# Performance work log

Measured on AMD Instinct MI355X. Metric: run time of the kernel, lower is better.

The kernel has to match this reference:

```python
import jax, jax.numpy as jnp
import numpy as np

B, T, DIM = 4, 2048, 1024
H, DH = 16, 64  # num_heads, dim_head; weight_dim = H*DH = 1024
SCALE = DIM ** (-0.5)  # note: original scales by dim**-0.5, not dim_head**-0.5


def setup_inputs() -> dict:
    key = jax.random.key(0)
    k1, k2, k3 = jax.random.split(key, 3)
    x = jax.random.normal(k1, (B, T, DIM), dtype=jnp.float32)
    w_qkv = jax.random.normal(k2, (3 * H * DH, DIM), dtype=jnp.float32) * (DIM ** -0.5)
    w_out = jax.random.normal(k3, (DIM, H * DH), dtype=jnp.float32) * ((H * DH) ** -0.5)
    b_out = jnp.zeros((DIM,), dtype=jnp.float32)
    return {"x": x, "w_qkv": w_qkv, "w_out": w_out, "b_out": b_out}


def reference(x, w_qkv, w_out, b_out):
    # qkv: [b, t, 3*H*DH] (torch Linear: x @ W^T)
    qkv = jnp.einsum('btc,oc->bto', x, w_qkv)
    # rearrange 'b t (d k h) -> k b h t d' with k=3, h=H: d is the OUTERMOST
    # factor of the flattened axis, then k, then h (h fastest-varying).
    qkv = qkv.reshape(B, T, DH, 3, H)          # [b, t, d, k, h]
    qkv = jnp.transpose(qkv, (3, 0, 4, 1, 2))   # [k, b, h, t, d]
    q, k, v = qkv[0], qkv[1], qkv[2]
    # scores: [b, h, t, t]
    attn = jnp.einsum('bhid,bhjd->bhij', q, k) * SCALE
    attn = jax.nn.softmax(attn, axis=-1)
    out = jnp.einsum('bhij,bhjd->bhid', attn, v)           # [b, h, t, d]
    out = jnp.transpose(out, (0, 2, 1, 3)).reshape(B, T, H * DH)  # 'b h t d -> b t (h d)'
    return jnp.einsum('btc,oc->bto', out, w_out) + b_out
```

## Files before the change

### kernel.cpp

```cpp
#include <hip/hip_runtime.h>
#include <hip/hip_bf16.h>


typedef __attribute__((ext_vector_type(8))) short short8;
typedef __attribute__((ext_vector_type(4))) float floatx4;

static __device__ __forceinline__ floatx4 mfma16(short8 a, short8 b, floatx4 c) {
    return __builtin_amdgcn_mfma_f32_16x16x32_bf16(a, b, c, 0, 0, 0);
}

static __device__ __forceinline__ unsigned short f2bf_bits(float f) {
    __hip_bfloat16 h = __float2bfloat16(f);
    return *reinterpret_cast<unsigned short*>(&h);
}

static __device__ __forceinline__ float fast_exp2(float x) {
#if __has_builtin(__builtin_amdgcn_exp2f)
    return __builtin_amdgcn_exp2f(x);
#else
    return exp2f(x);
#endif
}

#define GLD16(gptr, ldsptr)                                                  \
    __builtin_amdgcn_global_load_lds(                                        \
        (const __attribute__((address_space(1))) void*)(gptr),               \
        (__attribute__((address_space(3))) void*)(ldsptr), 16, 0, 0)

__global__ __launch_bounds__(256) void k_cvt(
    const float* __restrict__ src, unsigned short* __restrict__ dst, int n4)
{
    typedef __attribute__((ext_vector_type(4))) unsigned short ushort4v;
    for (int i = blockIdx.x * blockDim.x + threadIdx.x; i < n4;
         i += gridDim.x * blockDim.x) {
        const float4 v = ((const float4*)src)[i];
        ushort4v o;
        o.x = f2bf_bits(v.x);
        o.y = f2bf_bits(v.y);
        o.z = f2bf_bits(v.z);
        o.w = f2bf_bits(v.w);
        ((ushort4v*)dst)[i] = o;
    }
}

__global__ __launch_bounds__(256) void k_qkv(
    const unsigned short* __restrict__ x,
    const unsigned short* __restrict__ wq,
    unsigned short* __restrict__ qb,
    unsigned short* __restrict__ kb,
    unsigned short* __restrict__ vb)
{
    __shared__ unsigned short As[128 * 32];
    __shared__ unsigned short Bs[128 * 32];

    const int tid  = threadIdx.x;
    const int wave = tid >> 6, lane = tid & 63;
    const int quad = lane >> 4, l16 = lane & 15;
    const int wm = wave >> 1, wn = wave & 1;
    const int m0 = blockIdx.y * 128;
    const int kk = blockIdx.x >> 3;
    const int d0 = (blockIdx.x & 7) * 8;
    const int kkh = kk * 16;

    const int srow = lane >> 2;
    const int sc8  = (lane & 3) * 8;
    const int row0 = wave * 32 + srow;
    const int row1 = row0 + 16;
    const int bn0  = (d0 + (row0 >> 4)) * 48 + kkh + (row0 & 15);
    const int bn1  = (d0 + (row1 >> 4)) * 48 + kkh + (row1 & 15);

    floatx4 acc[4][4];
#pragma unroll
    for (int i = 0; i < 4; i++)
#pragma unroll
        for (int j = 0; j < 4; j++) acc[i][j] = (floatx4){0.f, 0.f, 0.f, 0.f};

    for (int k0 = 0; k0 < 1024; k0 += 32) {
        GLD16(&x[(m0 + row0) * 1024 + k0 + sc8], &As[(wave * 32) * 32]);
        GLD16(&x[(m0 + row1) * 1024 + k0 + sc8], &As[(wave * 32 + 16) * 32]);
        GLD16(&wq[bn0 * 1024 + k0 + sc8],        &Bs[(wave * 32) * 32]);
        GLD16(&wq[bn1 * 1024 + k0 + sc8],        &Bs[(wave * 32 + 16) * 32]);
        __syncthreads();

        short8 af[4], bfv[4];
#pragma unroll
        for (int mi = 0; mi < 4; mi++)
            af[mi] = *(const short8*)&As[(wm * 64 + mi * 16 + l16) * 32 + quad * 8];
#pragma unroll
        for (int ni = 0; ni < 4; ni++)
            bfv[ni] = *(const short8*)&Bs[(wn * 64 + ni * 16 + l16) * 32 + quad * 8];
#pragma unroll
        for (int mi = 0; mi < 4; mi++)
#pragma unroll
            for (int ni = 0; ni < 4; ni++)
                acc[mi][ni] = mfma16(af[mi], bfv[ni], acc[mi][ni]);
        __syncthreads();
    }

    unsigned short* dst = (kk == 0) ? qb : (kk == 1) ? kb : vb;
    const float scale = (kk == 0) ? 0.045084220027780106f : 1.0f;
#pragma unroll
    for (int ni = 0; ni < 4; ni++) {
        const int d = d0 + wn * 4 + ni;
#pragma unroll
        for (int mi = 0; mi < 4; mi++) {
            const int m  = m0 + wm * 64 + mi * 16 + quad * 4;
            const int b  = m >> 11;
            const int tt = m & 2047;
            ushort4 pk;
            pk.x = f2bf_bits(acc[mi][ni][0] * scale);
            pk.y = f2bf_bits(acc[mi][ni][1] * scale);
            pk.z = f2bf_bits(acc[mi][ni][2] * scale);
            pk.w = f2bf_bits(acc[mi][ni][3] * scale);
            *(ushort4*)&dst[((b * 16 + l16) * 64 + d) * 2048 + tt] = pk;
        }
    }
}

__global__ __launch_bounds__(256) void k_tr(
    const unsigned short* __restrict__ src,
    unsigned short* __restrict__ dst)
{
    __shared__ unsigned short Ts[64 * 72];
    const int tid = threadIdx.x;
    const int bh  = blockIdx.y;
    const int t0  = blockIdx.x * 64;
    const int dg  = (tid >> 4) * 4;
    const int tg  = (tid & 15) * 4;

    ushort4 rv[4];
#pragma unroll
    for (int dd = 0; dd < 4; dd++)
        rv[dd] = *(const ushort4*)&src[(bh * 64 + dg + dd) * 2048 + t0 + tg];
#pragma unroll
    for (int tt = 0; tt < 4; tt++) {
        ushort4 wv;
        wv.x = ((const unsigned short*)&rv[0])[tt];
        wv.y = ((const unsigned short*)&rv[1])[tt];
        wv.z = ((const unsigned short*)&rv[2])[tt];
        wv.w = ((const unsigned short*)&rv[3])[tt];
        *(ushort4*)&Ts[(tg + tt) * 72 + dg] = wv;
    }
    __syncthreads();

    const int tr = tid >> 2;
    const int c8 = (tid & 3) * 8;
    *(uint4*)&dst[(bh * 2048 + t0 + tr) * 64 + c8]      = *(const uint4*)&Ts[tr * 72 + c8];
    *(uint4*)&dst[(bh * 2048 + t0 + tr) * 64 + c8 + 32] = *(const uint4*)&Ts[tr * 72 + c8 + 32];
}

__global__ __launch_bounds__(512) void k_attn(
    const unsigned short* __restrict__ qt,
    const unsigned short* __restrict__ kt,
    const unsigned short* __restrict__ vg,
    __hip_bfloat16* __restrict__ og)
{
    __shared__ unsigned short Ks[64 * 72];
    __shared__ unsigned short Vt[64 * 72];
    __shared__ unsigned short Pt[8 * 32 * 72];

    const int tid  = threadIdx.x;
    const int wave = tid >> 6, lane = tid & 63;
    const int quad = lane >> 4, l16 = lane & 15;
    const int blk = blockIdx.x;
    const int bh  = (blk & 7) | ((blk >> 6) << 3);
    const int q0  = ((blk >> 3) & 7) * 256;
    const int qr  = q0 + wave * 32;

    short8 qf[2][2];
#pragma unroll
    for (int mi = 0; mi < 2; mi++)
#pragma unroll
        for (int ks = 0; ks < 2; ks++)
            qf[mi][ks] = *(const short8*)&qt[(bh * 2048 + qr + mi * 16 + l16) * 64 + ks * 32 + quad * 8];

    float lsum[2] = {0.f, 0.f};
    floatx4 o[2][4];
#pragma unroll
    for (int mi = 0; mi < 2; mi++)
#pragma unroll
        for (int di = 0; di < 4; di++) o[mi][di] = (floatx4){0.f, 0.f, 0.f, 0.f};

    const int srow = tid >> 3;
    const int sc8  = (tid & 7) * 8;

    for (int j0 = 0; j0 < 2048; j0 += 64) {
        *(uint4*)&Ks[srow * 72 + sc8] = *(const uint4*)&kt[(bh * 2048 + j0 + srow) * 64 + sc8];
        *(uint4*)&Vt[srow * 72 + sc8] = *(const uint4*)&vg[(bh * 64 + srow) * 2048 + j0 + sc8];
        __syncthreads();

        floatx4 st[2][4];
#pragma unroll
        for (int mi = 0; mi < 2; mi++)
#pragma unroll
            for (int nk = 0; nk < 4; nk++) st[mi][nk] = (floatx4){0.f, 0.f, 0.f, 0.f};
#pragma unroll
        for (int ks = 0; ks < 2; ks++) {
            short8 kf[4];
#pragma unroll
            for (int nk = 0; nk < 4; nk++)
                kf[nk] = *(const short8*)&Ks[(nk * 16 + l16) * 72 + ks * 32 + quad * 8];
#pragma unroll
            for (int mi = 0; mi < 2; mi++)
#pragma unroll
                for (int nk = 0; nk < 4; nk++)
                    st[mi][nk] = mfma16(kf[nk], qf[mi][ks], st[mi][nk]);
        }

#pragma unroll
        for (int mi = 0; mi < 2; mi++) {
#pragma unroll
            for (int nk = 0; nk < 4; nk++) {
                const float p0 = fast_exp2(st[mi][nk][0]);
                const float p1 = fast_exp2(st[mi][nk][1]);
                const float p2 = fast_exp2(st[mi][nk][2]);
                const float p3 = fast_exp2(st[mi][nk][3]);
                lsum[mi] += (p0 + p1) + (p2 + p3);
                ushort4 pk;
                pk.x = f2bf_bits(p0);
                pk.y = f2bf_bits(p1);
                pk.z = f2bf_bits(p2);
                pk.w = f2bf_bits(p3);
                *(ushort4*)&Pt[(wave * 32 + mi * 16 + l16) * 72 + nk * 16 + quad * 4] = pk;
            }
        }
        __builtin_amdgcn_s_waitcnt(0xc07f);

#pragma unroll
        for (int ks = 0; ks < 2; ks++) {
            short8 pf[2], vf[4];
#pragma unroll
            for (int mi = 0; mi < 2; mi++)
                pf[mi] = *(const short8*)&Pt[(wave * 32 + mi * 16 + l16) * 72 + ks * 32 + quad * 8];
#pragma unroll
            for (int di = 0; di < 4; di++)
                vf[di] = *(const short8*)&Vt[(di * 16 + l16) * 72 + ks * 32 + quad * 8];
#pragma unroll
            for (int mi = 0; mi < 2; mi++)
#pragma unroll
                for (int di = 0; di < 4; di++)
                    o[mi][di] = mfma16(pf[mi], vf[di], o[mi][di]);
        }
        __syncthreads();
    }

#pragma unroll
    for (int mi = 0; mi < 2; mi++) {
        float t = lsum[mi];
        t += __shfl_xor(t, 16);
        t += __shfl_xor(t, 32);
        lsum[mi] = t;
    }

    const int b = bh >> 4, h = bh & 15;
#pragma unroll
    for (int mi = 0; mi < 2; mi++) {
#pragma unroll
        for (int r = 0; r < 4; r++) {
            const float inv = 1.0f / __shfl(lsum[mi], quad * 4 + r);
            const int t = qr + mi * 16 + quad * 4 + r;
#pragma unroll
            for (int di = 0; di < 4; di++)
                og[(b * 2048 + t) * 1024 + h * 64 + di * 16 + l16] =
                    __float2bfloat16(o[mi][di][r] * inv);
        }
    }
}

__global__ __launch_bounds__(256) void k_out(
    const unsigned short* __restrict__ a,
    const unsigned short* __restrict__ wq,
    const float* __restrict__ bias,
    float* __restrict__ out)
{
    __shared__ unsigned short As[128 * 32];
    __shared__ unsigned short Bs[128 * 32];

    const int tid  = threadIdx.x;
    const int wave = tid >> 6, lane = tid & 63;
    const int quad = lane >> 4, l16 = lane & 15;
    const int wm = wave >> 1, wn = wave & 1;
    const int m0 = blockIdx.y * 128, n0 = blockIdx.x * 128;

    const int srow = lane >> 2;
    const int sc8  = (lane & 3) * 8;
    const int row0 = wave * 32 + srow;
    const int row1 = row0 + 16;

    floatx4 acc[4][4];
#pragma unroll
    for (int i = 0; i < 4; i++)
#pragma unroll
        for (int j = 0; j < 4; j++) acc[i][j] = (floatx4){0.f, 0.f, 0.f, 0.f};

    for (int k0 = 0; k0 < 1024; k0 += 32) {
        GLD16(&a[(m0 + row0) * 1024 + k0 + sc8],  &As[(wave * 32) * 32]);
        GLD16(&a[(m0 + row1) * 1024 + k0 + sc8],  &As[(wave * 32 + 16) * 32]);
        GLD16(&wq[(n0 + row0) * 1024 + k0 + sc8], &Bs[(wave * 32) * 32]);
        GLD16(&wq[(n0 + row1) * 1024 + k0 + sc8], &Bs[(wave * 32 + 16) * 32]);
        __syncthreads();

        short8 af[4], bfv[4];
#pragma unroll
        for (int mi = 0; mi < 4; mi++)
            af[mi] = *(const short8*)&As[(wm * 64 + mi * 16 + l16) * 32 + quad * 8];
#pragma unroll
        for (int ni = 0; ni < 4; ni++)
            bfv[ni] = *(const short8*)&Bs[(wn * 64 + ni * 16 + l16) * 32 + quad * 8];
#pragma unroll
        for (int mi = 0; mi < 4; mi++)
#pragma unroll
            for (int ni = 0; ni < 4; ni++)
                acc[mi][ni] = mfma16(af[mi], bfv[ni], acc[mi][ni]);
        __syncthreads();
    }

#pragma unroll
    for (int ni = 0; ni < 4; ni++) {
        const int col = n0 + wn * 64 + ni * 16 + l16;
        const float bv = bias[col];
#pragma unroll
        for (int mi = 0; mi < 4; mi++) {
            const int mbase = m0 + wm * 64 + mi * 16 + quad * 4;
#pragma unroll
            for (int r = 0; r < 4; r++)
                out[(mbase + r) * 1024 + col] = acc[mi][ni][r] + bv;
        }
    }
}

extern "C" void kernel_launch(void* const* d_in, const int* in_sizes, int n_in,
                              void* d_out, int out_size, void* d_ws, size_t ws_size,
                              hipStream_t stream) {
    const float* x    = (const float*)d_in[0];
    const float* wqkv = (const float*)d_in[1];
    const float* wout = (const float*)d_in[2];
    const float* bout = (const float*)d_in[3];
    float* out = (float*)d_out;

    unsigned short* ws = (unsigned short*)d_ws;
    unsigned short* xb    = ws;
    unsigned short* wqkvb = xb + 8388608;
    unsigned short* woutb = wqkvb + 3145728;
    unsigned short* qb    = woutb + 1048576;
    unsigned short* kb    = qb + 8388608;
    unsigned short* vb    = kb + 8388608;
    unsigned short* ob    = vb + 8388608;

    k_cvt<<<2048, 256, 0, stream>>>(x,    xb,    8388608 / 4);
    k_cvt<<<1024, 256, 0, stream>>>(wqkv, wqkvb, 3145728 / 4);
    k_cvt<<<512,  256, 0, stream>>>(wout, woutb, 1048576 / 4);

    k_qkv<<<dim3(24, 64), 256, 0, stream>>>(xb, wqkvb, qb, kb, vb);

    k_tr<<<dim3(32, 64), 256, 0, stream>>>(qb, xb);
    k_tr<<<dim3(32, 64), 256, 0, stream>>>(kb, qb);

    k_attn<<<512, 512, 0, stream>>>(xb, qb, vb, (__hip_bfloat16*)ob);
    k_out<<<dim3(8, 64), 256, 0, stream>>>(ob, woutb, bout, out);
}
```

Baseline: 309.8 us.

## Fuse Q/K transposes into QKV GEMM epilogue and double-size attention KV tiles

The QKV GEMM now picks weight rows per head so each block produces whole heads for Q and K. It writes them directly in [bh, t, d] layout through an LDS-staged transposed epilogue, which removes the two separate transpose kernels and their global round trips. The attention kernel loads 128-key tiles with register prefetch of the next tile, so global loads overlap compute and there are half as many barriers. It also raises wave priority around the MFMA blocks. The cost is more LDS use, extra barriers in the GEMM epilogue, and more register pressure in attention.

```diff
diff --git a/kernel.cpp b/kernel.cpp
--- a/kernel.cpp
+++ b/kernel.cpp
@@ -50,8 +50,7 @@
     unsigned short* __restrict__ kb,
     unsigned short* __restrict__ vb)
 {
-    __shared__ unsigned short As[128 * 32];
-    __shared__ unsigned short Bs[128 * 32];
+    __shared__ unsigned short SM[9216];
 
     const int tid  = threadIdx.x;
     const int wave = tid >> 6, lane = tid & 63;
@@ -59,15 +58,20 @@
     const int wm = wave >> 1, wn = wave & 1;
     const int m0 = blockIdx.y * 128;
     const int kk = blockIdx.x >> 3;
-    const int d0 = (blockIdx.x & 7) * 8;
-    const int kkh = kk * 16;
+    const int cb = blockIdx.x & 7;
 
     const int srow = lane >> 2;
     const int sc8  = (lane & 3) * 8;
     const int row0 = wave * 32 + srow;
     const int row1 = row0 + 16;
-    const int bn0  = (d0 + (row0 >> 4)) * 48 + kkh + (row0 & 15);
-    const int bn1  = (d0 + (row1 >> 4)) * 48 + kkh + (row1 & 15);
+    int bn0, bn1;
+    if (kk < 2) {
+        bn0 = (row0 & 63) * 48 + kk * 16 + cb * 2 + (row0 >> 6);
+        bn1 = (row1 & 63) * 48 + kk * 16 + cb * 2 + (row1 >> 6);
+    } else {
+        bn0 = (cb * 8 + (row0 >> 4)) * 48 + 32 + (row0 & 15);
+        bn1 = (cb * 8 + (row1 >> 4)) * 48 + 32 + (row1 & 15);
+    }
 
     floatx4 acc[4][4];
 #pragma unroll
@@ -76,19 +80,19 @@
         for (int j = 0; j < 4; j++) acc[i][j] = (floatx4){0.f, 0.f, 0.f, 0.f};
 
     for (int k0 = 0; k0 < 1024; k0 += 32) {
-        GLD16(&x[(m0 + row0) * 1024 + k0 + sc8], &As[(wave * 32) * 32]);
-        GLD16(&x[(m0 + row1) * 1024 + k0 + sc8], &As[(wave * 32 + 16) * 32]);
-        GLD16(&wq[bn0 * 1024 + k0 + sc8],        &Bs[(wave * 32) * 32]);
-        GLD16(&wq[bn1 * 1024 + k0 + sc8],        &Bs[(wave * 32 + 16) * 32]);
+        GLD16(&x[(m0 + row0) * 1024 + k0 + sc8], &SM[(wave * 32) * 32]);
+        GLD16(&x[(m0 + row1) * 1024 + k0 + sc8], &SM[(wave * 32 + 16) * 32]);
+        GLD16(&wq[bn0 * 1024 + k0 + sc8],        &SM[4096 + (wave * 32) * 32]);
+        GLD16(&wq[bn1 * 1024 + k0 + sc8],        &SM[4096 + (wave * 32 + 16) * 32]);
         __syncthreads();
 
         short8 af[4], bfv[4];
 #pragma unroll
         for (int mi = 0; mi < 4; mi++)
-            af[mi] = *(const short8*)&As[(wm * 64 + mi * 16 + l16) * 32 + quad * 8];
+            af[mi] = *(const short8*)&SM[(wm * 64 + mi * 16 + l16) * 32 + quad * 8];
 #pragma unroll
         for (int ni = 0; ni < 4; ni++)
-            bfv[ni] = *(const short8*)&Bs[(wn * 64 + ni * 16 + l16) * 32 + quad * 8];
+            bfv[ni] = *(const short8*)&SM[4096 + (wn * 64 + ni * 16 + l16) * 32 + quad * 8];
 #pragma unroll
         for (int mi = 0; mi < 4; mi++)
 #pragma unroll
@@ -97,56 +101,54 @@
         __syncthreads();
     }
 
-    unsigned short* dst = (kk == 0) ? qb : (kk == 1) ? kb : vb;
-    const float scale = (kk == 0) ? 0.045084220027780106f : 1.0f;
-#pragma unroll
-    for (int ni = 0; ni < 4; ni++) {
-        const int d = d0 + wn * 4 + ni;
-#pragma unroll
-        for (int mi = 0; mi < 4; mi++) {
-            const int m  = m0 + wm * 64 + mi * 16 + quad * 4;
-            const int b  = m >> 11;
-            const int tt = m & 2047;
-            ushort4 pk;
-            pk.x = f2bf_bits(acc[mi][ni][0] * scale);
-            pk.y = f2bf_bits(acc[mi][ni][1] * scale);
-            pk.z = f2bf_bits(acc[mi][ni][2] * scale);
-            pk.w = f2bf_bits(acc[mi][ni][3] * scale);
-            *(ushort4*)&dst[((b * 16 + l16) * 64 + d) * 2048 + tt] = pk;
-        }
-    }
-}
-
-__global__ __launch_bounds__(256) void k_tr(
-    const unsigned short* __restrict__ src,
-    unsigned short* __restrict__ dst)
-{
-    __shared__ unsigned short Ts[64 * 72];
-    const int tid = threadIdx.x;
-    const int bh  = blockIdx.y;
-    const int t0  = blockIdx.x * 64;
-    const int dg  = (tid >> 4) * 4;
-    const int tg  = (tid & 15) * 4;
-
-    ushort4 rv[4];
-#pragma unroll
-    for (int dd = 0; dd < 4; dd++)
-        rv[dd] = *(const ushort4*)&src[(bh * 64 + dg + dd) * 2048 + t0 + tg];
-#pragma unroll
-    for (int tt = 0; tt < 4; tt++) {
-        ushort4 wv;
-        wv.x = ((const unsigned short*)&rv[0])[tt];
-        wv.y = ((const unsigned short*)&rv[1])[tt];
-        wv.z = ((const unsigned short*)&rv[2])[tt];
-        wv.w = ((const unsigned short*)&rv[3])[tt];
-        *(ushort4*)&Ts[(tg + tt) * 72 + dg] = wv;
-    }
-    __syncthreads();
-
-    const int tr = tid >> 2;
-    const int c8 = (tid & 3) * 8;
-    *(uint4*)&dst[(bh * 2048 + t0 + tr) * 64 + c8]      = *(const uint4*)&Ts[tr * 72 + c8];
-    *(uint4*)&dst[(bh * 2048 + t0 + tr) * 64 + c8 + 32] = *(const uint4*)&Ts[tr * 72 + c8 + 32];
+    if (kk == 2) {
+#pragma unroll
+        for (int ni = 0; ni < 4; ni++) {
+            const int d = cb * 8 + wn * 4 + ni;
+#pragma unroll
+            for (int mi = 0; mi < 4; mi++) {
+                const int m  = m0 + wm * 64 + mi * 16 + quad * 4;
+                const int b  = m >> 11;
+                const int tt = m & 2047;
+                ushort4 pk;
+                pk.x = f2bf_bits(acc[mi][ni][0]);
+                pk.y = f2bf_bits(acc[mi][ni][1]);
+                pk.z = f2bf_bits(acc[mi][ni][2]);
+                pk.w = f2bf_bits(acc[mi][ni][3]);
+                *(ushort4*)&vb[((b * 16 + l16) * 64 + d) * 2048 + tt] = pk;
+            }
+        }
+    } else {
+        const float scale = (kk == 0) ? 0.045084220027780106f : 1.0f;
+        unsigned short* dst = (kk == 0) ? qb : kb;
+        const int b = m0 >> 11, tt0 = m0 & 2047;
+#pragma unroll
+        for (int s = 0; s < 2; s++) {
+            if (wn == s) {
+#pragma unroll
+                for (int ni = 0; ni < 4; ni++) {
+                    const int d = ni * 16 + l16;
+#pragma unroll
+                    for (int mi = 0; mi < 4; mi++) {
+                        const int tl = wm * 64 + mi * 16 + quad * 4;
+#pragma unroll
+                        for (int r = 0; r < 4; r++)
+                            SM[(tl + r) * 72 + d] = f2bf_bits(acc[mi][ni][r] * scale);
+                    }
+                }
+            }
+            __syncthreads();
+#pragma unroll
+            for (int u = 0; u < 4; u++) {
+                const int w  = tid + u * 256;
+                const int tl = w >> 3;
+                const int ch = (w & 7) * 8;
+                *(uint4*)&dst[((b * 16 + cb * 2 + s) * 2048 + tt0 + tl) * 64 + ch] =
+                    *(const uint4*)&SM[tl * 72 + ch];
+            }
+            __syncthreads();
+        }
+    }
 }
 
 __global__ __launch_bounds__(512) void k_attn(
@@ -155,8 +157,8 @@
     const unsigned short* __restrict__ vg,
     __hip_bfloat16* __restrict__ og)
 {
-    __shared__ unsigned short Ks[64 * 72];
-    __shared__ unsigned short Vt[64 * 72];
+    __shared__ unsigned short Ks[128 * 72];
+    __shared__ unsigned short Vt[64 * 136];
     __shared__ unsigned short Pt[8 * 32 * 72];
 
     const int tid  = threadIdx.x;
@@ -181,65 +183,87 @@
 #pragma unroll
         for (int di = 0; di < 4; di++) o[mi][di] = (floatx4){0.f, 0.f, 0.f, 0.f};
 
-    const int srow = tid >> 3;
-    const int sc8  = (tid & 7) * 8;
-
-    for (int j0 = 0; j0 < 2048; j0 += 64) {
-        *(uint4*)&Ks[srow * 72 + sc8] = *(const uint4*)&kt[(bh * 2048 + j0 + srow) * 64 + sc8];
-        *(uint4*)&Vt[srow * 72 + sc8] = *(const uint4*)&vg[(bh * 64 + srow) * 2048 + j0 + sc8];
-        __syncthreads();
-
-        floatx4 st[2][4];
-#pragma unroll
-        for (int mi = 0; mi < 2; mi++)
-#pragma unroll
-            for (int nk = 0; nk < 4; nk++) st[mi][nk] = (floatx4){0.f, 0.f, 0.f, 0.f};
-#pragma unroll
-        for (int ks = 0; ks < 2; ks++) {
-            short8 kf[4];
-#pragma unroll
-            for (int nk = 0; nk < 4; nk++)
-                kf[nk] = *(const short8*)&Ks[(nk * 16 + l16) * 72 + ks * 32 + quad * 8];
+    const int kr = tid >> 3, kc = (tid & 7) * 8;
+    const int vd = tid >> 4, vc = (tid & 15) * 8;
+
+    uint4 rk0 = *(const uint4*)&kt[(bh * 2048 + kr) * 64 + kc];
+    uint4 rk1 = *(const uint4*)&kt[(bh * 2048 + 64 + kr) * 64 + kc];
+    uint4 rv0 = *(const uint4*)&vg[(bh * 64 + vd) * 2048 + vc];
+    uint4 rv1 = *(const uint4*)&vg[(bh * 64 + 32 + vd) * 2048 + vc];
+
+    for (int j0 = 0; j0 < 2048; j0 += 128) {
+        *(uint4*)&Ks[kr * 72 + kc]         = rk0;
+        *(uint4*)&Ks[(64 + kr) * 72 + kc]  = rk1;
+        *(uint4*)&Vt[vd * 136 + vc]        = rv0;
+        *(uint4*)&Vt[(32 + vd) * 136 + vc] = rv1;
+        __syncthreads();
+        if (j0 + 128 < 2048) {
+            rk0 = *(const uint4*)&kt[(bh * 2048 + j0 + 128 + kr) * 64 + kc];
+            rk1 = *(const uint4*)&kt[(bh * 2048 + j0 + 192 + kr) * 64 + kc];
+            rv0 = *(const uint4*)&vg[(bh * 64 + vd) * 2048 + j0 + 128 + vc];
+            rv1 = *(const uint4*)&vg[(bh * 64 + 32 + vd) * 2048 + j0 + 128 + vc];
+        }
+
+#pragma unroll
+        for (int jj = 0; jj < 2; jj++) {
+            const int kb0 = jj * 64;
+
+            floatx4 st[2][4];
 #pragma unroll
             for (int mi = 0; mi < 2; mi++)
 #pragma unroll
+                for (int nk = 0; nk < 4; nk++) st[mi][nk] = (floatx4){0.f, 0.f, 0.f, 0.f};
+#pragma unroll
+            for (int ks = 0; ks < 2; ks++) {
+                short8 kf[4];
+#pragma unroll
                 for (int nk = 0; nk < 4; nk++)
-                    st[mi][nk] = mfma16(kf[nk], qf[mi][ks], st[mi][nk]);
-        }
-
-#pragma unroll
-        for (int mi = 0; mi < 2; mi++) {
-#pragma unroll
-            for (int nk = 0; nk < 4; nk++) {
-                const float p0 = fast_exp2(st[mi][nk][0]);
-                const float p1 = fast_exp2(st[mi][nk][1]);
-                const float p2 = fast_exp2(st[mi][nk][2]);
-                const float p3 = fast_exp2(st[mi][nk][3]);
-                lsum[mi] += (p0 + p1) + (p2 + p3);
-                ushort4 pk;
-                pk.x = f2bf_bits(p0);
-                pk.y = f2bf_bits(p1);
-                pk.z = f2bf_bits(p2);
-                pk.w = f2bf_bits(p3);
-                *(ushort4*)&Pt[(wave * 32 + mi * 16 + l16) * 72 + nk * 16 + quad * 4] = pk;
-            }
-        }
-        __builtin_amdgcn_s_waitcnt(0xc07f);
-
-#pragma unroll
-        for (int ks = 0; ks < 2; ks++) {
-            short8 pf[2], vf[4];
-#pragma unroll
-            for (int mi = 0; mi < 2; mi++)
-                pf[mi] = *(const short8*)&Pt[(wave * 32 + mi * 16 + l16) * 72 + ks * 32 + quad * 8];
-#pragma unroll
-            for (int di = 0; di < 4; di++)
-                vf[di] = *(const short8*)&Vt[(di * 16 + l16) * 72 + ks * 32 + quad * 8];
-#pragma unroll
-            for (int mi = 0; mi < 2; mi++)
+                    kf[nk] = *(const short8*)&Ks[(kb0 + nk * 16 + l16) * 72 + ks * 32 + quad * 8];
+                __builtin_amdgcn_s_setprio(1);
+#pragma unroll
+                for (int mi = 0; mi < 2; mi++)
+#pragma unroll
+                    for (int nk = 0; nk < 4; nk++)
+                        st[mi][nk] = mfma16(kf[nk], qf[mi][ks], st[mi][nk]);
+                __builtin_amdgcn_s_setprio(0);
+            }
+
+#pragma unroll
+            for (int mi = 0; mi < 2; mi++) {
+#pragma unroll
+                for (int nk = 0; nk < 4; nk++) {
+                    const float p0 = fast_exp2(st[mi][nk][0]);
+                    const float p1 = fast_exp2(st[mi][nk][1]);
+                    const float p2 = fast_exp2(st[mi][nk][2]);
+                    const float p3 = fast_exp2(st[mi][nk][3]);
+                    lsum[mi] += (p0 + p1) + (p2 + p3);
+                    ushort4 pk;
+                    pk.x = f2bf_bits(p0);
+                    pk.y = f2bf_bits(p1);
+                    pk.z = f2bf_bits(p2);
+                    pk.w = f2bf_bits(p3);
+                    *(ushort4*)&Pt[(wave * 32 + mi * 16 + l16) * 72 + nk * 16 + quad * 4] = pk;
+                }
+            }
+            __builtin_amdgcn_s_waitcnt(0xc07f);
+
+#pragma unroll
+            for (int ks = 0; ks < 2; ks++) {
+                short8 pf[2], vf[4];
+#pragma unroll
+                for (int mi = 0; mi < 2; mi++)
+                    pf[mi] = *(const short8*)&Pt[(wave * 32 + mi * 16 + l16) * 72 + ks * 32 + quad * 8];
 #pragma unroll
                 for (int di = 0; di < 4; di++)
-                    o[mi][di] = mfma16(pf[mi], vf[di], o[mi][di]);
+                    vf[di] = *(const short8*)&Vt[(di * 16 + l16) * 136 + kb0 + ks * 32 + quad * 8];
+                __builtin_amdgcn_s_setprio(1);
+#pragma unroll
+                for (int mi = 0; mi < 2; mi++)
+#pragma unroll
+                    for (int di = 0; di < 4; di++)
+                        o[mi][di] = mfma16(pf[mi], vf[di], o[mi][di]);
+                __builtin_amdgcn_s_setprio(0);
+            }
         }
         __syncthreads();
     }
@@ -352,10 +376,6 @@
     k_cvt<<<512,  256, 0, stream>>>(wout, woutb, 1048576 / 4);
 
     k_qkv<<<dim3(24, 64), 256, 0, stream>>>(xb, wqkvb, qb, kb, vb);
-
-    k_tr<<<dim3(32, 64), 256, 0, stream>>>(qb, xb);
-    k_tr<<<dim3(32, 64), 256, 0, stream>>>(kb, qb);
-
-    k_attn<<<512, 512, 0, stream>>>(xb, qb, vb, (__hip_bfloat16*)ob);
+    k_attn<<<512, 512, 0, stream>>>(qb, kb, vb, (__hip_bfloat16*)ob);
     k_out<<<dim3(8, 64), 256, 0, stream>>>(ob, woutb, bout, out);
 }
```

New measurement: 342.7 us. 10.6% more time.
